# Kernel tuning notes

Hardware: AMD Instinct MI355X
Metric: run time of the kernel (lower is better)

## Reference

```python
import jax, jax.numpy as jnp
import numpy as np

EPS = 1e-5
B, CIN, L = 512, 5, 1024   # batch, input channels, msp length == d_model
COUT, A, NB = 32, 13, 5    # CNN branch channels, max_atoms, num_bonds_prediction


def conv1d(x, w, pad, groups=1):
    # x: (N, C, L), w: (O, I/groups, K)
    return jax.lax.conv_general_dilated(
        x, w, window_strides=(1,), padding=[(pad, pad)],
        dimension_numbers=("NCH", "OIH", "NCH"), feature_group_count=groups)


def batchnorm(x, g, b):
    # training-mode BN over (N, L) per channel, as nn.BatchNorm1d in train()
    m = jnp.mean(x, axis=(0, 2), keepdims=True)
    v = jnp.var(x, axis=(0, 2), keepdims=True)
    return (x - m) * jax.lax.rsqrt(v + EPS) * g[None, :, None] + b[None, :, None]


def setup_inputs() -> dict:
    key = jax.random.key(0)
    ks = jax.random.split(key, 16)
    n = jax.random.normal
    inp = {
        "src": n(ks[0], (B, CIN, L), dtype=jnp.float32),
        "mask": jnp.ones((B, A), dtype=bool),
        "max_atoms": A,
        # CNN branch 1 (kernel 5) : depthwise, pointwise, BN, residual 1x1 conv
        "dw1": n(ks[1], (CIN, 1, 5), dtype=jnp.float32) * 0.2,
        "pw1": n(ks[2], (COUT, CIN, 1), dtype=jnp.float32) * 0.2,
        "g1": jnp.ones((COUT,), jnp.float32),
        "be1": jnp.zeros((COUT,), jnp.float32),
        "r1w": n(ks[3], (COUT, CIN, 1), dtype=jnp.float32) * 0.2,
        "r1b": jnp.zeros((COUT,), jnp.float32),
        # CNN branch 2 (kernel 3)
        "dw2": n(ks[4], (CIN, 1, 3), dtype=jnp.float32) * 0.2,
        "pw2": n(ks[5], (COUT, CIN, 1), dtype=jnp.float32) * 0.2,
        "g2": jnp.ones((COUT,), jnp.float32),
        "be2": jnp.zeros((COUT,), jnp.float32),
        "r2w": n(ks[6], (COUT, CIN, 1), dtype=jnp.float32) * 0.2,
        "r2b": jnp.zeros((COUT,), jnp.float32),
        # EdgeClassify2 linears: ll1 (2*COUT -> A), fl (2*L -> NB)
        "ll1w": n(ks[7], (A, 2 * COUT), dtype=jnp.float32) * 0.1,
        "ll1b": jnp.zeros((A,), jnp.float32),
        "flw": n(ks[8], (NB, 2 * L), dtype=jnp.float32) * 0.02,
        "flb": jnp.zeros((NB,), jnp.float32),
    }
    return inp


def reference(src, mask, max_atoms, dw1, pw1, g1, be1, r1w, r1b,
              dw2, pw2, g2, be2, r2w, r2b, ll1w, ll1b, flw, flb):
    # ---- CNN encoder ----
    e1 = jax.nn.relu(batchnorm(conv1d(conv1d(src, dw1, 2, groups=CIN), pw1, 0), g1, be1))
    e1 = e1 * (conv1d(src, r1w, 0) + r1b[None, :, None])
    e2 = jax.nn.relu(batchnorm(conv1d(conv1d(src, dw2, 1, groups=CIN), pw2, 0), g2, be2))
    e2 = e2 * (conv1d(src, r2w, 0) + r2b[None, :, None])
    x = jnp.concatenate([e1, e2], axis=1)          # (B, 2*COUT, L)
    # ---- EdgeClassify2 ----
    # ll1 over channel dim: (B, 2*COUT, L) -> (B, A, L)
    h = jnp.einsum("bcl,ac->bal", x, ll1w) + ll1b[None, :, None]
    # vectorized replacement of the O(A^2) python loop:
    # final_e[:, i, j] = concat(h[:, min(i,j)], h[:, max(i,j)])
    idx = jnp.arange(max_atoms)
    mn = jnp.minimum(idx[:, None], idx[None, :])   # (A, A)
    mx = jnp.maximum(idx[:, None], idx[None, :])
    final_e = jnp.concatenate([h[:, mn, :], h[:, mx, :]], axis=-1)  # (B, A, A, 2L)
    out = jnp.einsum("bijd,nd->bijn", final_e, flw) + flb           # (B, A, A, NB)
    return out
```

## Files before the change

### kernel.cpp

```cpp
#include <hip/hip_runtime.h>
#include <hip/hip_bf16.h>

#define BB 512
#define LL 1024
#define AA 13
#define NBP 5
#define NTOT (BB * LL)
#define EPSV 1e-5f

#define WS_F     192
#define WS_PART  256
#define WS_CONST 10496

template<int CTRL, int RM, bool BC>
__device__ __forceinline__ float dppadd(float v) {
    int t = __builtin_amdgcn_update_dpp(0, __float_as_int(v), CTRL, RM, 0xf, BC);
    return v + __int_as_float(t);
}
__device__ __forceinline__ float wave_sum(float v) {
    v = dppadd<0x111, 0xf, true >(v);
    v = dppadd<0x112, 0xf, true >(v);
    v = dppadd<0x114, 0xf, true >(v);
    v = dppadd<0x118, 0xf, true >(v);
    v = dppadd<0x142, 0xa, false>(v);
    v = dppadd<0x143, 0xc, false>(v);
    return v;
}

__global__ __launch_bounds__(256) void k_moments(
    const float* __restrict__ src,
    const float* __restrict__ dw1,
    const float* __restrict__ dw2,
    const float* __restrict__ flw,
    float* __restrict__ ws)
{
    __shared__ float red[4][40];
    __shared__ float fred[4];
    int tid = threadIdx.x;
    int gid = blockIdx.x * 256 + tid;
    int b = gid >> 7, L0 = (gid & 127) << 3;
    const float* sb = src + b * (5 * LL);

    float w1[5][5], w2[5][3];
#pragma unroll
    for (int c = 0; c < 5; c++) {
#pragma unroll
        for (int t = 0; t < 5; t++) w1[c][t] = dw1[c*5+t];
#pragma unroll
        for (int t = 0; t < 3; t++) w2[c][t] = dw2[c*3+t];
    }

    float x[5][16];
#pragma unroll
    for (int c5 = 0; c5 < 5; c5++) {
        const float* sp = sb + c5 * LL;
        float4 xa = (L0 >= 4)    ? *(const float4*)(sp + L0 - 4) : make_float4(0,0,0,0);
        float4 xb = *(const float4*)(sp + L0);
        float4 xc = *(const float4*)(sp + L0 + 4);
        float4 xd = (L0 <= 1012) ? *(const float4*)(sp + L0 + 8) : make_float4(0,0,0,0);
        x[c5][0]=xa.x; x[c5][1]=xa.y; x[c5][2]=xa.z; x[c5][3]=xa.w;
        x[c5][4]=xb.x; x[c5][5]=xb.y; x[c5][6]=xb.z; x[c5][7]=xb.w;
        x[c5][8]=xc.x; x[c5][9]=xc.y; x[c5][10]=xc.z; x[c5][11]=xc.w;
        x[c5][12]=xd.x; x[c5][13]=xd.y; x[c5][14]=xd.z; x[c5][15]=xd.w;
    }

    float acc[40];
#pragma unroll
    for (int k = 0; k < 40; k++) acc[k] = 0.f;

#pragma unroll
    for (int k = 0; k < 8; k++) {
        float d1[5], d2[5];
#pragma unroll
        for (int c5 = 0; c5 < 5; c5++) {
            d1[c5] = w1[c5][0]*x[c5][k+2] + w1[c5][1]*x[c5][k+3] + w1[c5][2]*x[c5][k+4]
                   + w1[c5][3]*x[c5][k+5] + w1[c5][4]*x[c5][k+6];
            d2[c5] = w2[c5][0]*x[c5][k+3] + w2[c5][1]*x[c5][k+4] + w2[c5][2]*x[c5][k+5];
        }
#pragma unroll
        for (int j = 0; j < 5; j++) { acc[j] += d1[j]; acc[20+j] += d2[j]; }
#pragma unroll
        for (int j = 0; j < 5; j++)
#pragma unroll
            for (int kk = j; kk < 5; kk++) {
                int idx = j*(11-j)/2 + (kk - j);
                acc[5+idx]  += d1[j]*d1[kk];
                acc[25+idx] += d2[j]*d2[kk];
            }
    }

    int lane = tid & 63, wv = tid >> 6;
#pragma unroll
    for (int k = 0; k < 40; k++) acc[k] = wave_sum(acc[k]);
    if (lane == 63) {
#pragma unroll
        for (int k = 0; k < 40; k++) red[wv][k] = acc[k];
    }
    __syncthreads();
    if (tid < 40) {
        ws[WS_PART + blockIdx.x * 40 + tid] =
            red[0][tid] + red[1][tid] + red[2][tid] + red[3][tid];
    }

    if (blockIdx.x < 10) {
        int nn = blockIdx.x;
        int n = nn < 5 ? nn : nn - 5;
        int off = nn < 5 ? 0 : LL;
        float4 v = *(const float4*)(flw + n * (2*LL) + off + tid * 4);
        float s = wave_sum(v.x + v.y + v.z + v.w);
        if (lane == 63) fred[wv] = s;
        __syncthreads();
        if (tid == 0) ws[WS_F + nn] = fred[0] + fred[1] + fred[2] + fred[3];
    }
}

__global__ __launch_bounds__(320) void k_prep(
    float* __restrict__ ws,
    const float* __restrict__ pw1, const float* __restrict__ pw2,
    const float* __restrict__ g1,  const float* __restrict__ be1,
    const float* __restrict__ g2,  const float* __restrict__ be2,
    const float* __restrict__ r1w, const float* __restrict__ r2w,
    const float* __restrict__ r1b, const float* __restrict__ r2b)
{
    __shared__ float momS[40];
    int tid = threadIdx.x;
    {
        int k = tid >> 3, sub = tid & 7;
        float v = 0.f;
#pragma unroll 8
        for (int t2 = 0; t2 < 32; t2++) v += ws[WS_PART + (sub + (t2 << 3)) * 40 + k];
        v += __shfl_xor(v, 1, 64);
        v += __shfl_xor(v, 2, 64);
        v += __shfl_xor(v, 4, 64);
        if (sub == 0) momS[k] = v;
    }
    __syncthreads();
    if (tid < 64) {
        int brc = tid >> 5, o = tid & 31;
        const float invN = 1.0f / (float)NTOT;
        const float* pw = brc ? pw2 : pw1;
        const float* rw = brc ? r2w : r1w;
        const float* s  = momS + (brc ? 20 : 0);
        const float* M  = momS + (brc ? 25 : 5);
        float pwv[5], rwv[5], md[5];
#pragma unroll
        for (int j = 0; j < 5; j++) { pwv[j] = pw[o*5+j]; rwv[j] = rw[o*5+j]; md[j] = s[j] * invN; }
        float meanY = 0.f;
#pragma unroll
        for (int j = 0; j < 5; j++) meanY += pwv[j] * md[j];
        float ey2 = 0.f;
#pragma unroll
        for (int j = 0; j < 5; j++)
#pragma unroll
            for (int k = 0; k < 5; k++) {
                int lo = j < k ? j : k, hi = j < k ? k : j;
                int idx = lo*(11-lo)/2 + (hi - lo);
                ey2 += pwv[j] * pwv[k] * (M[idx] * invN);
            }
        float varY = ey2 - meanY * meanY;
        if (varY < 0.f) varY = 0.f;
        float gg = brc ? g2[o] : g1[o];
        float bb = brc ? be2[o] : be1[o];
        float rb = brc ? r2b[o] : r1b[o];
        float sc = gg * rsqrtf(varY + EPSV);
        float sh = bb - meanY * sc;
        float* dst = ws + WS_CONST + tid * 16;
        dst[0] = pwv[0]*sc; dst[1] = pwv[1]*sc; dst[2] = pwv[2]*sc; dst[3] = pwv[3]*sc;
        dst[4] = pwv[4]*sc; dst[5] = sh;        dst[6] = rb;        dst[7] = 0.f;
        dst[8] = rwv[0];    dst[9] = rwv[1];    dst[10] = rwv[2];   dst[11] = rwv[3];
        dst[12] = rwv[4];   dst[13] = 0.f;      dst[14] = 0.f;      dst[15] = 0.f;
    }
}

__global__ __launch_bounds__(512, 2) void k_fused(
    const float* __restrict__ src,
    const float* __restrict__ dw1,
    const float* __restrict__ dw2,
    const float* __restrict__ flw,
    const float* __restrict__ ll1w,
    const float* __restrict__ ll1b,
    const float* __restrict__ flb,
    const float* __restrict__ ws,
    float* __restrict__ out)
{
    __shared__ __align__(16) float srcS[5][1040];
    __shared__ __align__(16) float SLds[64][12];
    __shared__ float llT[832];
    __shared__ float PQ[130];

    int tid = threadIdx.x, b = blockIdx.x;
    int lane = tid & 63;
    int gu = __builtin_amdgcn_readfirstlane(tid >> 6);
    int br = gu >> 2;

    const float* srcB = src + b * (5 * LL);

    for (int idx = tid; idx < 5 * 256; idx += 512) {
        int c5 = idx >> 8, q = idx & 255;
        float4 v = *(const float4*)(srcB + (c5 << 10) + (q << 2));
        *(float4*)&srcS[c5][(q << 2) + 8] = v;
    }
    if (tid < 40) {
        int c5 = tid >> 3, j = tid & 7;
        int i = (j < 4) ? (4 + j) : (1028 + j);
        srcS[c5][i] = 0.f;
    }
    for (int idx = tid; idx < 832; idx += 512) {
        int cc = idx / 13, a = idx - cc * 13;
        llT[idx] = ll1w[a * 64 + cc];
    }
    __syncthreads();

    float wdw[5][5];
    if (br == 0) {
#pragma unroll
        for (int c5 = 0; c5 < 5; c5++)
#pragma unroll
            for (int t = 0; t < 5; t++) wdw[c5][t] = dw1[c5*5+t];
    } else {
#pragma unroll
        for (int c5 = 0; c5 < 5; c5++) {
            wdw[c5][0] = 0.f;
            wdw[c5][1] = dw2[c5*3+0]; wdw[c5][2] = dw2[c5*3+1]; wdw[c5][3] = dw2[c5*3+2];
            wdw[c5][4] = 0.f;
        }
    }
    const float* cb = ws + WS_CONST + (gu << 7);

    float acc[80];
#pragma unroll
    for (int k = 0; k < 80; k++) acc[k] = 0.f;
    int c0 = gu << 3;

#pragma unroll 1
    for (int p = 0; p < 4; p++) {
        int l0 = (p << 8) + (lane << 2);
        float fwv[10][4];
#pragma unroll
        for (int nn = 0; nn < 10; nn++) {
            int n = nn < 5 ? nn : nn - 5;
            int off = nn < 5 ? 0 : LL;
            float4 t4 = *(const float4*)(flw + n * (2*LL) + off + l0);
            fwv[nn][0] = t4.x; fwv[nn][1] = t4.y; fwv[nn][2] = t4.z; fwv[nn][3] = t4.w;
        }
        float dv[5][4], sv[5][4];
#pragma unroll
        for (int c5 = 0; c5 < 5; c5++) {
            int i0 = l0 + 8;
            float4 xa = *(const float4*)&srcS[c5][i0 - 4];
            float4 xb = *(const float4*)&srcS[c5][i0];
            float4 xc = *(const float4*)&srcS[c5][i0 + 4];
            float xx[12] = {xa.x, xa.y, xa.z, xa.w, xb.x, xb.y, xb.z, xb.w, xc.x, xc.y, xc.z, xc.w};
            sv[c5][0] = xb.x; sv[c5][1] = xb.y; sv[c5][2] = xb.z; sv[c5][3] = xb.w;
            if (br == 0) {
#pragma unroll
                for (int q = 0; q < 4; q++)
                    dv[c5][q] = wdw[c5][0]*xx[q+2] + wdw[c5][1]*xx[q+3] + wdw[c5][2]*xx[q+4]
                              + wdw[c5][3]*xx[q+5] + wdw[c5][4]*xx[q+6];
            } else {
#pragma unroll
                for (int q = 0; q < 4; q++)
                    dv[c5][q] = wdw[c5][1]*xx[q+3] + wdw[c5][2]*xx[q+4] + wdw[c5][3]*xx[q+5];
            }
        }
#pragma unroll
        for (int ci = 0; ci < 8; ci++) {
            const float4 A  = *(const float4*)(cb + ci*16);
            const float4 B2 = *(const float4*)(cb + ci*16 + 4);
            const float4 R0 = *(const float4*)(cb + ci*16 + 8);
            const float4 R1 = *(const float4*)(cb + ci*16 + 12);
            float e[4];
#pragma unroll
            for (int q = 0; q < 4; q++) {
                float y = B2.y + A.x*dv[0][q] + A.y*dv[1][q] + A.z*dv[2][q]
                                + A.w*dv[3][q] + B2.x*dv[4][q];
                float r = B2.z + R0.x*sv[0][q] + R0.y*sv[1][q] + R0.z*sv[2][q]
                                + R0.w*sv[3][q] + R1.x*sv[4][q];
                e[q] = fmaxf(y, 0.f) * r;
            }
#pragma unroll
            for (int nn = 0; nn < 10; nn++) {
                acc[ci*10 + nn] += e[0]*fwv[nn][0] + e[1]*fwv[nn][1]
                                 + e[2]*fwv[nn][2] + e[3]*fwv[nn][3];
            }
        }
    }

#pragma unroll
    for (int k = 0; k < 80; k++) acc[k] = wave_sum(acc[k]);
    if (lane == 63) {
#pragma unroll
        for (int ci = 0; ci < 8; ci++) {
            int c = c0 + ci;
            *(float4*)&SLds[c][0] = make_float4(acc[ci*10+0], acc[ci*10+1], acc[ci*10+2], acc[ci*10+3]);
            *(float4*)&SLds[c][4] = make_float4(acc[ci*10+4], acc[ci*10+5], acc[ci*10+6], acc[ci*10+7]);
            *(float2*)&SLds[c][8] = make_float2(acc[ci*10+8], acc[ci*10+9]);
        }
    }
    __syncthreads();

    if (tid < 130) {
        int half = tid >= 65 ? 1 : 0;
        int q = tid - half * 65;
        int a = q / 5, n = q - a * 5;
        int col = half * 5 + n;
        float v = ll1b[a] * ws[WS_F + col];
#pragma unroll 8
        for (int cc = 0; cc < 64; cc++) v += llT[cc * 13 + a] * SLds[cc][col];
        PQ[tid] = v;
    }
    __syncthreads();

    for (int idx = tid; idx < AA * AA * NBP; idx += 512) {
        int i = idx / 65;
        int rr = idx - i * 65;
        int j = rr / 5, n = rr - j * 5;
        int mn = i < j ? i : j, mx = i < j ? j : i;
        out[b * (AA * AA * NBP) + idx] = PQ[mn * 5 + n] + PQ[65 + mx * 5 + n] + flb[n];
    }
}

extern "C" void kernel_launch(void* const* d_in, const int* in_sizes, int n_in,
                              void* d_out, int out_size, void* d_ws, size_t ws_size,
                              hipStream_t stream) {
    const float* src  = (const float*)d_in[0];
    const float* dw1  = (const float*)d_in[3];
    const float* pw1  = (const float*)d_in[4];
    const float* g1   = (const float*)d_in[5];
    const float* be1  = (const float*)d_in[6];
    const float* r1w  = (const float*)d_in[7];
    const float* r1b  = (const float*)d_in[8];
    const float* dw2  = (const float*)d_in[9];
    const float* pw2  = (const float*)d_in[10];
    const float* g2   = (const float*)d_in[11];
    const float* be2  = (const float*)d_in[12];
    const float* r2w  = (const float*)d_in[13];
    const float* r2b  = (const float*)d_in[14];
    const float* ll1w = (const float*)d_in[15];
    const float* ll1b = (const float*)d_in[16];
    const float* flw  = (const float*)d_in[17];
    const float* flb  = (const float*)d_in[18];
    float* ws  = (float*)d_ws;
    float* out = (float*)d_out;

    k_moments<<<256, 256, 0, stream>>>(src, dw1, dw2, flw, ws);
    k_prep<<<1, 320, 0, stream>>>(ws, pw1, pw2, g1, be1, g2, be2, r1w, r2w, r1b, r2b);
    k_fused<<<BB, 512, 0, stream>>>(src, dw1, dw2, flw, ll1w, ll1b, flb, ws, out);
}
```

Baseline: 153.6 us.

## Compute flw projection with split-bf16 MFMA instead of scalar FMAs and wave reductions

Rewrites the fused kernel's projection of the activation map onto the ten fl-weight rows as a matrix multiply. Each block now runs 1024 threads, each wave computing 4 channels. The activation tile is written to swizzled LDS as high/low bf16 pairs and multiplied by split-bf16 weights using three MFMA 16x16x32 ops per k-step, which keeps roughly fp32 accuracy. This replaces the 80-register accumulators and DPP wave reductions, but adds LDS staging, extra barriers per pass, and a cross-wave partial-sum reduction.

Result: faster. 142.4 us (-7.3%).

```diff
diff --git a/kernel.cpp b/kernel.cpp
--- a/kernel.cpp
+++ b/kernel.cpp
@@ -11,6 +11,9 @@
 #define WS_F     192
 #define WS_PART  256
 #define WS_CONST 10496
+
+typedef __attribute__((ext_vector_type(8))) short bhalf8;
+typedef __attribute__((ext_vector_type(4))) float floatx4;
 
 template<int CTRL, int RM, bool BC>
 __device__ __forceinline__ float dppadd(float v) {
@@ -172,7 +175,7 @@
     }
 }
 
-__global__ __launch_bounds__(512, 2) void k_fused(
+__global__ __launch_bounds__(1024, 1) void k_fused(
     const float* __restrict__ src,
     const float* __restrict__ dw1,
     const float* __restrict__ dw2,
@@ -184,18 +187,20 @@
     float* __restrict__ out)
 {
     __shared__ __align__(16) float srcS[5][1040];
-    __shared__ __align__(16) float SLds[64][12];
     __shared__ float llT[832];
+    __shared__ __align__(16) unsigned int eBuf[16384];
+    __shared__ __align__(16) float Sarr[1024];
     __shared__ float PQ[130];
 
     int tid = threadIdx.x, b = blockIdx.x;
     int lane = tid & 63;
     int gu = __builtin_amdgcn_readfirstlane(tid >> 6);
-    int br = gu >> 2;
+    int br = gu >> 3;
+    int c0 = gu << 2;
 
     const float* srcB = src + b * (5 * LL);
 
-    for (int idx = tid; idx < 5 * 256; idx += 512) {
+    for (int idx = tid; idx < 5 * 256; idx += 1024) {
         int c5 = idx >> 8, q = idx & 255;
         float4 v = *(const float4*)(srcB + (c5 << 10) + (q << 2));
         *(float4*)&srcS[c5][(q << 2) + 8] = v;
@@ -205,11 +210,10 @@
         int i = (j < 4) ? (4 + j) : (1028 + j);
         srcS[c5][i] = 0.f;
     }
-    for (int idx = tid; idx < 832; idx += 512) {
+    for (int idx = tid; idx < 832; idx += 1024) {
         int cc = idx / 13, a = idx - cc * 13;
         llT[idx] = ll1w[a * 64 + cc];
     }
-    __syncthreads();
 
     float wdw[5][5];
     if (br == 0) {
@@ -225,77 +229,141 @@
             wdw[c5][4] = 0.f;
         }
     }
-    const float* cb = ws + WS_CONST + (gu << 7);
-
-    float acc[80];
-#pragma unroll
-    for (int k = 0; k < 80; k++) acc[k] = 0.f;
-    int c0 = gu << 3;
+    const float* cb = ws + WS_CONST + (c0 << 4);
+
+    int mt  = gu & 3;
+    int ks0 = (gu >> 2) << 1;
+    floatx4 Cacc = {0.f, 0.f, 0.f, 0.f};
+
+    int nB = lane & 15;
+    int kg = (lane >> 4) << 3;
+    const float* fbase = flw + (nB % 5) * 2048 + (nB / 5) * 1024;
+
+    __syncthreads();
 
 #pragma unroll 1
-    for (int p = 0; p < 4; p++) {
+    for (int p = 0; p < 4; ++p) {
+        float fv[2][8];
+        {
+            int gl0 = (p << 8) + (ks0 << 5) + kg;
+            if (nB < 10) {
+                float4 a0 = *(const float4*)(fbase + gl0);
+                float4 a1 = *(const float4*)(fbase + gl0 + 4);
+                float4 b0 = *(const float4*)(fbase + gl0 + 32);
+                float4 b1 = *(const float4*)(fbase + gl0 + 36);
+                fv[0][0]=a0.x; fv[0][1]=a0.y; fv[0][2]=a0.z; fv[0][3]=a0.w;
+                fv[0][4]=a1.x; fv[0][5]=a1.y; fv[0][6]=a1.z; fv[0][7]=a1.w;
+                fv[1][0]=b0.x; fv[1][1]=b0.y; fv[1][2]=b0.z; fv[1][3]=b0.w;
+                fv[1][4]=b1.x; fv[1][5]=b1.y; fv[1][6]=b1.z; fv[1][7]=b1.w;
+            } else {
+#pragma unroll
+                for (int j = 0; j < 8; j++) { fv[0][j] = 0.f; fv[1][j] = 0.f; }
+            }
+        }
+
         int l0 = (p << 8) + (lane << 2);
-        float fwv[10][4];
-#pragma unroll
-        for (int nn = 0; nn < 10; nn++) {
-            int n = nn < 5 ? nn : nn - 5;
-            int off = nn < 5 ? 0 : LL;
-            float4 t4 = *(const float4*)(flw + n * (2*LL) + off + l0);
-            fwv[nn][0] = t4.x; fwv[nn][1] = t4.y; fwv[nn][2] = t4.z; fwv[nn][3] = t4.w;
-        }
         float dv[5][4], sv[5][4];
-#pragma unroll
-        for (int c5 = 0; c5 < 5; c5++) {
+        {
             int i0 = l0 + 8;
-            float4 xa = *(const float4*)&srcS[c5][i0 - 4];
-            float4 xb = *(const float4*)&srcS[c5][i0];
-            float4 xc = *(const float4*)&srcS[c5][i0 + 4];
-            float xx[12] = {xa.x, xa.y, xa.z, xa.w, xb.x, xb.y, xb.z, xb.w, xc.x, xc.y, xc.z, xc.w};
-            sv[c5][0] = xb.x; sv[c5][1] = xb.y; sv[c5][2] = xb.z; sv[c5][3] = xb.w;
-            if (br == 0) {
-#pragma unroll
-                for (int q = 0; q < 4; q++)
-                    dv[c5][q] = wdw[c5][0]*xx[q+2] + wdw[c5][1]*xx[q+3] + wdw[c5][2]*xx[q+4]
-                              + wdw[c5][3]*xx[q+5] + wdw[c5][4]*xx[q+6];
-            } else {
-#pragma unroll
-                for (int q = 0; q < 4; q++)
-                    dv[c5][q] = wdw[c5][1]*xx[q+3] + wdw[c5][2]*xx[q+4] + wdw[c5][3]*xx[q+5];
-            }
-        }
-#pragma unroll
-        for (int ci = 0; ci < 8; ci++) {
+#pragma unroll
+            for (int c5 = 0; c5 < 5; c5++) {
+                float4 xa = *(const float4*)&srcS[c5][i0 - 4];
+                float4 xb = *(const float4*)&srcS[c5][i0];
+                float4 xc = *(const float4*)&srcS[c5][i0 + 4];
+                float xx[12] = {xa.x, xa.y, xa.z, xa.w, xb.x, xb.y, xb.z, xb.w, xc.x, xc.y, xc.z, xc.w};
+                sv[c5][0] = xb.x; sv[c5][1] = xb.y; sv[c5][2] = xb.z; sv[c5][3] = xb.w;
+                if (br == 0) {
+#pragma unroll
+                    for (int q = 0; q < 4; q++)
+                        dv[c5][q] = wdw[c5][0]*xx[q+2] + wdw[c5][1]*xx[q+3] + wdw[c5][2]*xx[q+4]
+                                  + wdw[c5][3]*xx[q+5] + wdw[c5][4]*xx[q+6];
+                } else {
+#pragma unroll
+                    for (int q = 0; q < 4; q++)
+                        dv[c5][q] = wdw[c5][1]*xx[q+3] + wdw[c5][2]*xx[q+4] + wdw[c5][3]*xx[q+5];
+                }
+            }
+        }
+
+        char* eb = (char*)eBuf;
+#pragma unroll
+        for (int ci = 0; ci < 4; ci++) {
             const float4 A  = *(const float4*)(cb + ci*16);
             const float4 B2 = *(const float4*)(cb + ci*16 + 4);
             const float4 R0 = *(const float4*)(cb + ci*16 + 8);
             const float4 R1 = *(const float4*)(cb + ci*16 + 12);
-            float e[4];
-#pragma unroll
-            for (int q = 0; q < 4; q++) {
-                float y = B2.y + A.x*dv[0][q] + A.y*dv[1][q] + A.z*dv[2][q]
-                                + A.w*dv[3][q] + B2.x*dv[4][q];
-                float r = B2.z + R0.x*sv[0][q] + R0.y*sv[1][q] + R0.z*sv[2][q]
-                                + R0.w*sv[3][q] + R1.x*sv[4][q];
-                e[q] = fmaxf(y, 0.f) * r;
-            }
-#pragma unroll
-            for (int nn = 0; nn < 10; nn++) {
-                acc[ci*10 + nn] += e[0]*fwv[nn][0] + e[1]*fwv[nn][1]
-                                 + e[2]*fwv[nn][2] + e[3]*fwv[nn][3];
-            }
-        }
-    }
-
-#pragma unroll
-    for (int k = 0; k < 80; k++) acc[k] = wave_sum(acc[k]);
-    if (lane == 63) {
-#pragma unroll
-        for (int ci = 0; ci < 8; ci++) {
+            unsigned int hp[2], lp[2];
+#pragma unroll
+            for (int hq = 0; hq < 2; hq++) {
+                unsigned int hw[2], lw[2];
+#pragma unroll
+                for (int s = 0; s < 2; s++) {
+                    int q = hq * 2 + s;
+                    float y = B2.y + A.x*dv[0][q] + A.y*dv[1][q] + A.z*dv[2][q]
+                                    + A.w*dv[3][q] + B2.x*dv[4][q];
+                    float r = B2.z + R0.x*sv[0][q] + R0.y*sv[1][q] + R0.z*sv[2][q]
+                                    + R0.w*sv[3][q] + R1.x*sv[4][q];
+                    float e = fmaxf(y, 0.f) * r;
+                    unsigned int u = __float_as_uint(e);
+                    hw[s] = u & 0xFFFF0000u;
+                    float lf = e - __uint_as_float(hw[s]);
+                    lw[s] = __float_as_uint(lf) & 0xFFFF0000u;
+                }
+                hp[hq] = (hw[0] >> 16) | hw[1];
+                lp[hq] = (lw[0] >> 16) | lw[1];
+            }
             int c = c0 + ci;
-            *(float4*)&SLds[c][0] = make_float4(acc[ci*10+0], acc[ci*10+1], acc[ci*10+2], acc[ci*10+3]);
-            *(float4*)&SLds[c][4] = make_float4(acc[ci*10+4], acc[ci*10+5], acc[ci*10+6], acc[ci*10+7]);
-            *(float2*)&SLds[c][8] = make_float2(acc[ci*10+8], acc[ci*10+9]);
-        }
+            int off = (c << 9) + (((lane << 3)) ^ ((c & 7) << 4));
+            *(uint2*)(eb + off)         = make_uint2(hp[0], hp[1]);
+            *(uint2*)(eb + 32768 + off) = make_uint2(lp[0], lp[1]);
+        }
+        __syncthreads();
+
+        {
+            int arow = (mt << 4) + (lane & 15);
+            int swz  = (arow & 7) << 4;
+            int rb2  = arow << 9;
+#pragma unroll
+            for (int kk = 0; kk < 2; kk++) {
+                int ksl = (ks0 + kk) << 5;
+                int kbyte = (((ksl + kg) << 1)) ^ swz;
+                bhalf8 aH = *(const bhalf8*)(eb + rb2 + kbyte);
+                bhalf8 aL = *(const bhalf8*)(eb + 32768 + rb2 + kbyte);
+                bhalf8 bH, bL;
+#pragma unroll
+                for (int j = 0; j < 8; j++) {
+                    float f = fv[kk][j];
+                    unsigned int u = __float_as_uint(f);
+                    unsigned int hu = u & 0xFFFF0000u;
+                    bH[j] = (short)(u >> 16);
+                    float lf = f - __uint_as_float(hu);
+                    bL[j] = (short)(__float_as_uint(lf) >> 16);
+                }
+                Cacc = __builtin_amdgcn_mfma_f32_16x16x32_bf16(aH, bH, Cacc, 0, 0, 0);
+                Cacc = __builtin_amdgcn_mfma_f32_16x16x32_bf16(aH, bL, Cacc, 0, 0, 0);
+                Cacc = __builtin_amdgcn_mfma_f32_16x16x32_bf16(aL, bH, Cacc, 0, 0, 0);
+            }
+        }
+        __syncthreads();
+    }
+
+    {
+        float* part = (float*)eBuf;
+        int basep = (gu << 8) + ((lane >> 4) << 6) + (lane & 15);
+        part[basep]      = Cacc[0];
+        part[basep + 16] = Cacc[1];
+        part[basep + 32] = Cacc[2];
+        part[basep + 48] = Cacc[3];
+    }
+    __syncthreads();
+    {
+        int c = tid >> 4, n = tid & 15;
+        int m = c >> 4, row = c & 15;
+        const float* part = (const float*)eBuf;
+        int o = (row << 4) + n;
+        float s = part[(m) * 256 + o] + part[(4 + m) * 256 + o]
+                + part[(8 + m) * 256 + o] + part[(12 + m) * 256 + o];
+        Sarr[tid] = s;
     }
     __syncthreads();
 
@@ -306,12 +374,12 @@
         int col = half * 5 + n;
         float v = ll1b[a] * ws[WS_F + col];
 #pragma unroll 8
-        for (int cc = 0; cc < 64; cc++) v += llT[cc * 13 + a] * SLds[cc][col];
+        for (int cc = 0; cc < 64; cc++) v += llT[cc * 13 + a] * Sarr[(cc << 4) + col];
         PQ[tid] = v;
     }
     __syncthreads();
 
-    for (int idx = tid; idx < AA * AA * NBP; idx += 512) {
+    for (int idx = tid; idx < AA * AA * NBP; idx += 1024) {
         int i = idx / 65;
         int rr = idx - i * 65;
         int j = rr / 5, n = rr - j * 5;
@@ -345,5 +413,5 @@
 
     k_moments<<<256, 256, 0, stream>>>(src, dw1, dw2, flw, ws);
     k_prep<<<1, 320, 0, stream>>>(ws, pw1, pw2, g1, be1, g2, be2, r1w, r2w, r1b, r2b);
-    k_fused<<<BB, 512, 0, stream>>>(src, dw1, dw2, flw, ll1w, ll1b, flb, ws, out);
-}
+    k_fused<<<BB, 1024, 0, stream>>>(src, dw1, dw2, flw, ll1w, ll1b, flb, ws, out);
+}
```

## Replace scalar flw reduction with split-bf16 MFMA over LDS-staged activations

Applied to the files above, without the earlier changes.

Moves the per-channel contraction of the encoder output against the final linear weights from scalar FMAs with wave reductions onto 16x16x32 bf16 MFMA instructions. Both operands are split into high and low bf16 parts (three MFMAs per step) to keep roughly fp32 accuracy. The weights are pre-split and packed in k_moments. Activations are staged in a 64KB swizzled LDS buffer each pass, and src is now read directly from global memory instead of being staged in LDS. This removes the 80-accumulator register pressure and the 80 wave_sum reductions, at the cost of extra LDS traffic, two barriers per pass, reduced occupancy from the large LDS buffer, and some precision loss.

New measurement: 147.6 us. 3.9% less time.

```diff
diff --git a/kernel.cpp b/kernel.cpp
--- a/kernel.cpp
+++ b/kernel.cpp
@@ -11,6 +11,19 @@
 #define WS_F     192
 #define WS_PART  256
 #define WS_CONST 10496
+#define WS_FLW   16384
+
+typedef __attribute__((ext_vector_type(8))) short bhalf8;
+typedef __attribute__((ext_vector_type(4))) float floatx4;
+
+__device__ __forceinline__ void trunc_pair(float e0, float e1, unsigned int& hp, unsigned int& lp) {
+    unsigned int u0 = __float_as_uint(e0), u1 = __float_as_uint(e1);
+    unsigned int h0 = u0 & 0xFFFF0000u, h1 = u1 & 0xFFFF0000u;
+    hp = (h0 >> 16) | h1;
+    float l0 = e0 - __uint_as_float(h0);
+    float l1 = e1 - __uint_as_float(h1);
+    lp = (__float_as_uint(l0) >> 16) | (__float_as_uint(l1) & 0xFFFF0000u);
+}
 
 template<int CTRL, int RM, bool BC>
 __device__ __forceinline__ float dppadd(float v) {
@@ -107,10 +120,23 @@
         int n = nn < 5 ? nn : nn - 5;
         int off = nn < 5 ? 0 : LL;
         float4 v = *(const float4*)(flw + n * (2*LL) + off + tid * 4);
+        {
+            unsigned int hp0, lp0, hp1, lp1;
+            trunc_pair(v.x, v.y, hp0, lp0);
+            trunc_pair(v.z, v.w, hp1, lp1);
+            char* fwb = (char*)(ws + WS_FLW);
+            *(uint2*)(fwb + nn * 2048 + tid * 8)         = make_uint2(hp0, hp1);
+            *(uint2*)(fwb + 32768 + nn * 2048 + tid * 8) = make_uint2(lp0, lp1);
+        }
         float s = wave_sum(v.x + v.y + v.z + v.w);
         if (lane == 63) fred[wv] = s;
         __syncthreads();
         if (tid == 0) ws[WS_F + nn] = fred[0] + fred[1] + fred[2] + fred[3];
+    } else if (blockIdx.x < 16) {
+        int nn = blockIdx.x;
+        char* fwb = (char*)(ws + WS_FLW);
+        *(uint2*)(fwb + nn * 2048 + tid * 8)         = make_uint2(0u, 0u);
+        *(uint2*)(fwb + 32768 + nn * 2048 + tid * 8) = make_uint2(0u, 0u);
     }
 }
 
@@ -176,40 +202,29 @@
     const float* __restrict__ src,
     const float* __restrict__ dw1,
     const float* __restrict__ dw2,
-    const float* __restrict__ flw,
     const float* __restrict__ ll1w,
     const float* __restrict__ ll1b,
     const float* __restrict__ flb,
-    const float* __restrict__ ws,
+    const float* __restrict__ ws_ro,
     float* __restrict__ out)
 {
-    __shared__ __align__(16) float srcS[5][1040];
-    __shared__ __align__(16) float SLds[64][12];
+    __shared__ __align__(16) char eBuf[65536];
     __shared__ float llT[832];
     __shared__ float PQ[130];
 
     int tid = threadIdx.x, b = blockIdx.x;
     int lane = tid & 63;
     int gu = __builtin_amdgcn_readfirstlane(tid >> 6);
+    int c0 = gu << 3;
     int br = gu >> 2;
+    int mt = gu & 3, kq = gu >> 2;
 
     const float* srcB = src + b * (5 * LL);
 
-    for (int idx = tid; idx < 5 * 256; idx += 512) {
-        int c5 = idx >> 8, q = idx & 255;
-        float4 v = *(const float4*)(srcB + (c5 << 10) + (q << 2));
-        *(float4*)&srcS[c5][(q << 2) + 8] = v;
-    }
-    if (tid < 40) {
-        int c5 = tid >> 3, j = tid & 7;
-        int i = (j < 4) ? (4 + j) : (1028 + j);
-        srcS[c5][i] = 0.f;
-    }
     for (int idx = tid; idx < 832; idx += 512) {
         int cc = idx / 13, a = idx - cc * 13;
         llT[idx] = ll1w[a * 64 + cc];
     }
-    __syncthreads();
 
     float wdw[5][5];
     if (br == 0) {
@@ -225,42 +240,43 @@
             wdw[c5][4] = 0.f;
         }
     }
-    const float* cb = ws + WS_CONST + (gu << 7);
-
-    float acc[80];
-#pragma unroll
-    for (int k = 0; k < 80; k++) acc[k] = 0.f;
-    int c0 = gu << 3;
+    const float* cb = ws_ro + WS_CONST + (c0 << 4);
+
+    int nB = lane & 15;
+    int kg = (lane >> 4) << 3;
+    const char* fwb = (const char*)(ws_ro + WS_FLW);
+    floatx4 Cacc = {0.f, 0.f, 0.f, 0.f};
 
 #pragma unroll 1
-    for (int p = 0; p < 4; p++) {
+    for (int p = 0; p < 4; ++p) {
+        uint4 bhv[4], blv[4];
+#pragma unroll
+        for (int k2 = 0; k2 < 4; ++k2) {
+            int lg = (p << 8) + (((kq << 2) + k2) << 5) + kg;
+            bhv[k2] = *(const uint4*)(fwb + (((nB << 10) + lg) << 1));
+            blv[k2] = *(const uint4*)(fwb + 32768 + (((nB << 10) + lg) << 1));
+        }
+
         int l0 = (p << 8) + (lane << 2);
-        float fwv[10][4];
-#pragma unroll
-        for (int nn = 0; nn < 10; nn++) {
-            int n = nn < 5 ? nn : nn - 5;
-            int off = nn < 5 ? 0 : LL;
-            float4 t4 = *(const float4*)(flw + n * (2*LL) + off + l0);
-            fwv[nn][0] = t4.x; fwv[nn][1] = t4.y; fwv[nn][2] = t4.z; fwv[nn][3] = t4.w;
-        }
         float dv[5][4], sv[5][4];
 #pragma unroll
         for (int c5 = 0; c5 < 5; c5++) {
-            int i0 = l0 + 8;
-            float4 xa = *(const float4*)&srcS[c5][i0 - 4];
-            float4 xb = *(const float4*)&srcS[c5][i0];
-            float4 xc = *(const float4*)&srcS[c5][i0 + 4];
-            float xx[12] = {xa.x, xa.y, xa.z, xa.w, xb.x, xb.y, xb.z, xb.w, xc.x, xc.y, xc.z, xc.w};
-            sv[c5][0] = xb.x; sv[c5][1] = xb.y; sv[c5][2] = xb.z; sv[c5][3] = xb.w;
+            const float* s5 = srcB + (c5 << 10);
+            float4 xa = (l0 >= 4)    ? *(const float4*)(s5 + l0 - 4) : make_float4(0,0,0,0);
+            float4 xb = *(const float4*)(s5 + l0);
+            float4 xc = (l0 <= 1016) ? *(const float4*)(s5 + l0 + 4) : make_float4(0,0,0,0);
+            float xx[8] = {xa.z, xa.w, xb.x, xb.y, xb.z, xb.w, xc.x, xc.y};
+#pragma unroll
+            for (int q = 0; q < 4; q++) sv[c5][q] = xx[q + 2];
             if (br == 0) {
 #pragma unroll
                 for (int q = 0; q < 4; q++)
-                    dv[c5][q] = wdw[c5][0]*xx[q+2] + wdw[c5][1]*xx[q+3] + wdw[c5][2]*xx[q+4]
-                              + wdw[c5][3]*xx[q+5] + wdw[c5][4]*xx[q+6];
+                    dv[c5][q] = wdw[c5][0]*xx[q] + wdw[c5][1]*xx[q+1] + wdw[c5][2]*xx[q+2]
+                              + wdw[c5][3]*xx[q+3] + wdw[c5][4]*xx[q+4];
             } else {
 #pragma unroll
                 for (int q = 0; q < 4; q++)
-                    dv[c5][q] = wdw[c5][1]*xx[q+3] + wdw[c5][2]*xx[q+4] + wdw[c5][3]*xx[q+5];
+                    dv[c5][q] = wdw[c5][1]*xx[q+1] + wdw[c5][2]*xx[q+2] + wdw[c5][3]*xx[q+3];
             }
         }
 #pragma unroll
@@ -278,24 +294,51 @@
                                 + R0.w*sv[3][q] + R1.x*sv[4][q];
                 e[q] = fmaxf(y, 0.f) * r;
             }
-#pragma unroll
-            for (int nn = 0; nn < 10; nn++) {
-                acc[ci*10 + nn] += e[0]*fwv[nn][0] + e[1]*fwv[nn][1]
-                                 + e[2]*fwv[nn][2] + e[3]*fwv[nn][3];
-            }
-        }
-    }
-
-#pragma unroll
-    for (int k = 0; k < 80; k++) acc[k] = wave_sum(acc[k]);
-    if (lane == 63) {
-#pragma unroll
-        for (int ci = 0; ci < 8; ci++) {
+            unsigned int hp0, lp0, hp1, lp1;
+            trunc_pair(e[0], e[1], hp0, lp0);
+            trunc_pair(e[2], e[3], hp1, lp1);
             int c = c0 + ci;
-            *(float4*)&SLds[c][0] = make_float4(acc[ci*10+0], acc[ci*10+1], acc[ci*10+2], acc[ci*10+3]);
-            *(float4*)&SLds[c][4] = make_float4(acc[ci*10+4], acc[ci*10+5], acc[ci*10+6], acc[ci*10+7]);
-            *(float2*)&SLds[c][8] = make_float2(acc[ci*10+8], acc[ci*10+9]);
-        }
+            int off = (c << 10) + ((lane << 3) ^ ((c & 7) << 4));
+            *(uint2*)(eBuf + off)       = make_uint2(hp0, hp1);
+            *(uint2*)(eBuf + off + 512) = make_uint2(lp0, lp1);
+        }
+        __syncthreads();
+
+        {
+            int ch   = (mt << 4) + (lane & 15);
+            int rowb = ch << 10;
+            int swz  = (ch & 7) << 4;
+#pragma unroll
+            for (int k2 = 0; k2 < 4; ++k2) {
+                int lbc = (((kq << 2) + k2) << 5) + kg;
+                bhalf8 aH = *(const bhalf8*)(eBuf + rowb + ((lbc << 1) ^ swz));
+                bhalf8 aL = *(const bhalf8*)(eBuf + rowb + 512 + ((lbc << 1) ^ swz));
+                union { uint4 u; bhalf8 v; } bh, bl;
+                bh.u = bhv[k2]; bl.u = blv[k2];
+                Cacc = __builtin_amdgcn_mfma_f32_16x16x32_bf16(aH, bh.v, Cacc, 0, 0, 0);
+                Cacc = __builtin_amdgcn_mfma_f32_16x16x32_bf16(aH, bl.v, Cacc, 0, 0, 0);
+                Cacc = __builtin_amdgcn_mfma_f32_16x16x32_bf16(aL, bh.v, Cacc, 0, 0, 0);
+            }
+        }
+        __syncthreads();
+    }
+
+    {
+        float* part = (float*)eBuf;
+        int basep = (gu << 8) + ((lane >> 4) << 6) + (lane & 15);
+        part[basep]      = Cacc[0];
+        part[basep + 16] = Cacc[1];
+        part[basep + 32] = Cacc[2];
+        part[basep + 48] = Cacc[3];
+    }
+    __syncthreads();
+    float* SarrF = (float*)eBuf + 4096;
+    for (int idx = tid; idx < 1024; idx += 512) {
+        int c = idx >> 4, n = idx & 15;
+        int mt2 = c >> 4, m = c & 15;
+        const float* part = (const float*)eBuf;
+        int o = (m << 4) + n;
+        SarrF[idx] = part[mt2 * 256 + o] + part[(4 + mt2) * 256 + o];
     }
     __syncthreads();
 
@@ -304,9 +347,9 @@
         int q = tid - half * 65;
         int a = q / 5, n = q - a * 5;
         int col = half * 5 + n;
-        float v = ll1b[a] * ws[WS_F + col];
+        float v = ll1b[a] * ws_ro[WS_F + col];
 #pragma unroll 8
-        for (int cc = 0; cc < 64; cc++) v += llT[cc * 13 + a] * SLds[cc][col];
+        for (int cc = 0; cc < 64; cc++) v += llT[cc * 13 + a] * SarrF[(cc << 4) + col];
         PQ[tid] = v;
     }
     __syncthreads();
@@ -345,5 +388,5 @@
 
     k_moments<<<256, 256, 0, stream>>>(src, dw1, dw2, flw, ws);
     k_prep<<<1, 320, 0, stream>>>(ws, pw1, pw2, g1, be1, g2, be2, r1w, r2w, r1b, r2b);
-    k_fused<<<BB, 512, 0, stream>>>(src, dw1, dw2, flw, ll1w, ll1b, flb, ws, out);
-}
+    k_fused<<<BB, 512, 0, stream>>>(src, dw1, dw2, ll1w, ll1b, flb, ws, out);
+}
```
